# Kernel optimization log

Hardware: AMD Instinct MI355X
Metric: run time of the kernel (lower is better)

## Reference

```python
import jax, jax.numpy as jnp
import numpy as np

# Module dims (match init_kwargs)
D_IN = 1024
N_PRI = 2048
D_PRI = 16
N_CLS = 25
D_CLS = 16
ITERS = 3
B = 64
EPS = 1e-6


def layer_norm(x, g, b, eps=1e-5):
    m = x.mean(-1, keepdims=True)
    v = ((x - m) ** 2).mean(-1, keepdims=True)
    return (x - m) / jnp.sqrt(v + eps) * g + b


def setup_inputs() -> dict:
    key = jax.random.key(0)
    ks = jax.random.split(key, 6)
    s = lambda n: 1.0 / np.sqrt(n)
    return {
        "z": jax.random.normal(ks[0], (B, D_IN), jnp.float32),
        # to_primary: Linear(d_in, n_primary*d_primary)
        "w1": jax.random.normal(ks[1], (D_IN, N_PRI * D_PRI), jnp.float32) * s(D_IN),
        "b1": jnp.zeros((N_PRI * D_PRI,), jnp.float32),
        # primary_act: LayerNorm(d_in) -> Linear(d_in, n_primary) -> Sigmoid
        "ln1_g": jnp.ones((D_IN,), jnp.float32),
        "ln1_b": jnp.zeros((D_IN,), jnp.float32),
        "w2": jax.random.normal(ks[2], (D_IN, N_PRI), jnp.float32) * s(D_IN),
        "b2": jnp.zeros((N_PRI,), jnp.float32),
        # CapsuleFC transform + EM routing params
        "w_caps": jax.random.normal(ks[3], (N_PRI, D_PRI, N_CLS, D_CLS), jnp.float32) * s(D_PRI),
        "beta_u": jnp.zeros((N_CLS,), jnp.float32),
        "beta_a": jnp.zeros((N_CLS,), jnp.float32),
        # to_logits: LayerNorm(d_class) -> Linear(d_class, 1)
        "ln2_g": jnp.ones((D_CLS,), jnp.float32),
        "ln2_b": jnp.zeros((D_CLS,), jnp.float32),
        "w3": jax.random.normal(ks[4], (D_CLS, 1), jnp.float32) * s(D_CLS),
        "b3": jnp.zeros((1,), jnp.float32),
    }


def em_routing(V, a_in, beta_u, beta_a, n_iter):
    # V: (b, n_in, n_out, d) votes; a_in: (b, n_in) primary activations
    b, n, o, d = V.shape
    R = jnp.full((b, n, o), 1.0 / o, V.dtype)  # routing assignments
    lam = jnp.asarray(1.0, V.dtype)            # inverse temperature
    for _ in range(n_iter):
        # M-step: weighted mean/variance per output capsule
        r = R * a_in[:, :, None]                                  # (b,n,o)
        r_sum = r.sum(axis=1) + EPS                               # (b,o)
        mu = jnp.einsum('bno,bnod->bod', r, V) / r_sum[..., None]  # (b,o,d)
        diff2 = (V - mu[:, None]) ** 2                            # (b,n,o,d)
        sigma2 = jnp.einsum('bno,bnod->bod', r, diff2) / r_sum[..., None] + EPS
        cost = (beta_u[None, :, None] + 0.5 * jnp.log(sigma2)) * r_sum[..., None]
        a_out = jax.nn.sigmoid(lam * (beta_a[None, :] - cost.sum(-1)))  # (b,o)
        # E-step: Gaussian log-likelihood of each vote under each output capsule
        logp = (-0.5 * (diff2 / sigma2[:, None]).sum(-1)
                - 0.5 * jnp.log(sigma2).sum(-1)[:, None, :])      # (b,n,o)
        R = jax.nn.softmax(jnp.log(a_out + EPS)[:, None, :] + logp, axis=-1)
    return mu, a_out, R


def reference(z, w1, b1, ln1_g, ln1_b, w2, b2, w_caps, beta_u, beta_a,
              ln2_g, ln2_b, w3, b3):
    b = z.shape[0]
    # primary poses (no squash: use_squash_primary=False)
    primary_pose = (z @ w1 + b1).reshape(b, N_PRI, D_PRI)
    # primary activations
    primary_act = jnp.clip(jax.nn.sigmoid(layer_norm(z, ln1_g, ln1_b) @ w2 + b2), 0.0, 1.0)
    # votes: each primary capsule predicts each class capsule's pose
    V = jnp.einsum('bni,niod->bnod', primary_pose, w_caps)  # (B, N_PRI, N_CLS, D_CLS)
    class_pose, class_act, q = em_routing(V, primary_act, beta_u, beta_a, ITERS)
    logits = (layer_norm(class_pose, ln2_g, ln2_b) @ w3 + b3).squeeze(-1)  # (B, N_CLS)
    acts = jnp.linalg.norm(class_pose, axis=-1)                            # (B, N_CLS)
    return logits, acts, class_pose, q
```

## Files before the change

kernel.cpp:

```cpp
#include <hip/hip_runtime.h>
#include <hip/hip_bf16.h>
#include <cstdio>

#define B     64
#define DIN   1024
#define NPRI  2048
#define DPRI  16
#define NCLS  25
#define DCLS  16
#define EMEPS 1e-6f
#define LNEPS 1e-5f
#define KS2   8
#define NCHUNK_S 16

#define OFF_POSE 0
#define OFF_ZN   (OFF_POSE + NPRI*DPRI*B)
#define OFF_ACTT (OFF_ZN + B*DIN)
#define OFF_G2P  (OFF_ACTT + NPRI*B)
#define OFF_V    (OFF_G2P + KS2*NPRI*B)
#define V_FLOATS (NPRI*NCLS*B*DCLS/2)
#define OFF_R    (OFF_V + V_FLOATS)
#define R_FLOATS (NPRI*NCLS*B/2)
#define OFF_PART (OFF_R + R_FLOATS)
#define OFF_STAT (OFF_PART + NCLS*NCHUNK_S*33*B)
#define OFF_MU   (OFF_STAT + NCLS*33*B)
#define OFF_MI4  (OFF_MU + NCLS*DCLS*B)
#define OFF_BASE (OFF_MI4 + NCLS*8*B*4)
#define WS_FLOATS (OFF_BASE + NCLS*B)

__device__ __forceinline__ unsigned pack_f16(float a, float b) {
  union { _Float16 h[2]; unsigned u; } x;
  x.h[0] = (_Float16)a; x.h[1] = (_Float16)b;
  return x.u;
}
__device__ __forceinline__ float f16lo(unsigned u) {
  union { unsigned u; _Float16 h[2]; } x; x.u = u; return (float)x.h[0];
}
__device__ __forceinline__ float f16hi(unsigned u) {
  union { unsigned u; _Float16 h[2]; } x; x.u = u; return (float)x.h[1];
}
__device__ __forceinline__ unsigned short f16bits(float a) {
  union { _Float16 h; unsigned short u; } x; x.h = (_Float16)a; return x.u;
}
__device__ __forceinline__ float f16val(unsigned short u) {
  union { unsigned short u; _Float16 h; } x; x.u = u; return (float)x.h;
}

__global__ __launch_bounds__(256) void k_ln(const float* __restrict__ z,
                                            const float* __restrict__ g,
                                            const float* __restrict__ bb,
                                            float* __restrict__ zn) {
  int row = blockIdx.x, t = threadIdx.x;
  const float* zr = z + row * DIN;
  float4 v = ((const float4*)zr)[t];
  float s  = v.x + v.y + v.z + v.w;
  float s2 = v.x*v.x + v.y*v.y + v.z*v.z + v.w*v.w;
  for (int off = 32; off; off >>= 1) {
    s  += __shfl_down(s, off);
    s2 += __shfl_down(s2, off);
  }
  __shared__ float ls[8];
  int wv = t >> 6, ln = t & 63;
  if (ln == 0) { ls[wv*2] = s; ls[wv*2+1] = s2; }
  __syncthreads();
  s  = ls[0] + ls[2] + ls[4] + ls[6];
  s2 = ls[1] + ls[3] + ls[5] + ls[7];
  float mean = s * (1.0f / DIN);
  float var  = s2 * (1.0f / DIN) - mean * mean;
  float inv  = 1.0f / sqrtf(var + LNEPS);
  float4 gg = ((const float4*)g)[t];
  float4 bv = ((const float4*)bb)[t];
  float4 o;
  o.x = (v.x - mean) * inv * gg.x + bv.x;
  o.y = (v.y - mean) * inv * gg.y + bv.y;
  o.z = (v.z - mean) * inv * gg.z + bv.z;
  o.w = (v.w - mean) * inv * gg.w + bv.w;
  ((float4*)(zn + row * DIN))[t] = o;
}

__global__ __launch_bounds__(256, 2) void k_gemm1(const float* __restrict__ z,
                                                  const float* __restrict__ w1,
                                                  const float* __restrict__ b1,
                                                  float* __restrict__ poseT) {
  __shared__ __align__(16) float zTl[128 * 68];
  __shared__ __align__(16) float wl[128 * 68];
  int t = threadIdx.x;
  int c0 = blockIdx.x * 64;

  int r0  = (t >> 4) * 4;
  int c0l = (t & 15) * 4;

  int zr_ = t >> 2, za = t & 3;
  int wk = t >> 1, wc = (t & 1) * 32;

  float acc[4][4];
#pragma unroll
  for (int j = 0; j < 4; ++j)
#pragma unroll
    for (int i = 0; i < 4; ++i) acc[j][i] = 0.f;

  for (int kc = 0; kc < 8; ++kc) {
    int k0 = kc * 128;
    __syncthreads();
#pragma unroll
    for (int jj = 0; jj < 4; ++jj) {
      int kb = za * 8 + jj * 32;
      const float* src = z + zr_ * DIN + k0 + kb;
      float4 v0 = *(const float4*)src;
      float4 v1 = *(const float4*)(src + 4);
      zTl[(kb+0)*68 + zr_] = v0.x; zTl[(kb+1)*68 + zr_] = v0.y;
      zTl[(kb+2)*68 + zr_] = v0.z; zTl[(kb+3)*68 + zr_] = v0.w;
      zTl[(kb+4)*68 + zr_] = v1.x; zTl[(kb+5)*68 + zr_] = v1.y;
      zTl[(kb+6)*68 + zr_] = v1.z; zTl[(kb+7)*68 + zr_] = v1.w;
    }
    const float* wsrc = w1 + (size_t)(k0 + wk) * 32768 + c0 + wc;
#pragma unroll
    for (int j = 0; j < 8; ++j)
      *(float4*)&wl[wk * 68 + wc + j * 4] = *(const float4*)(wsrc + j * 4);
    __syncthreads();

#pragma unroll 4
    for (int k = 0; k < 128; ++k) {
      float4 zr4 = *(const float4*)&zTl[k * 68 + r0];
      float4 wr4 = *(const float4*)&wl[k * 68 + c0l];
      float zz[4] = {zr4.x, zr4.y, zr4.z, zr4.w};
      float ww[4] = {wr4.x, wr4.y, wr4.z, wr4.w};
#pragma unroll
      for (int j = 0; j < 4; ++j)
#pragma unroll
        for (int i = 0; i < 4; ++i) acc[j][i] += ww[j] * zz[i];
    }
  }
#pragma unroll
  for (int j = 0; j < 4; ++j) {
    int c = c0 + c0l + j;
    float bc = b1[c];
    float4 o = {acc[j][0] + bc, acc[j][1] + bc, acc[j][2] + bc, acc[j][3] + bc};
    *(float4*)&poseT[c * 64 + r0] = o;
  }
}

__global__ __launch_bounds__(256, 2) void k_gemm2p(const float* __restrict__ zn,
                                                   const float* __restrict__ w2,
                                                   float* __restrict__ part) {
  __shared__ __align__(16) float znT[128 * 68];
  __shared__ __align__(16) float wl[128 * 68];
  int t = threadIdx.x;
  int c0 = blockIdx.x * 64;
  int k0 = blockIdx.y * 128;
  int zr_ = t >> 2, za = t & 3;
  int wk = t >> 1, wc = (t & 1) * 32;

#pragma unroll
  for (int jj = 0; jj < 4; ++jj) {
    int kb = za * 8 + jj * 32;
    const float* src = zn + zr_ * DIN + k0 + kb;
    float4 v0 = *(const float4*)src;
    float4 v1 = *(const float4*)(src + 4);
    znT[(kb+0)*68 + zr_] = v0.x; znT[(kb+1)*68 + zr_] = v0.y;
    znT[(kb+2)*68 + zr_] = v0.z; znT[(kb+3)*68 + zr_] = v0.w;
    znT[(kb+4)*68 + zr_] = v1.x; znT[(kb+5)*68 + zr_] = v1.y;
    znT[(kb+6)*68 + zr_] = v1.z; znT[(kb+7)*68 + zr_] = v1.w;
  }
  const float* wsrc = w2 + (size_t)(k0 + wk) * NPRI + c0 + wc;
#pragma unroll
  for (int j = 0; j < 8; ++j)
    *(float4*)&wl[wk * 68 + wc + j * 4] = *(const float4*)(wsrc + j * 4);
  __syncthreads();

  int r0 = (t >> 4) * 4, c0l = (t & 15) * 4;
  float acc[4][4];
#pragma unroll
  for (int j = 0; j < 4; ++j)
#pragma unroll
    for (int i = 0; i < 4; ++i) acc[j][i] = 0.f;

#pragma unroll 4
  for (int k = 0; k < 128; ++k) {
    float4 z4 = *(const float4*)&znT[k * 68 + r0];
    float4 w4 = *(const float4*)&wl[k * 68 + c0l];
    float zz[4] = {z4.x, z4.y, z4.z, z4.w};
    float ww[4] = {w4.x, w4.y, w4.z, w4.w};
#pragma unroll
    for (int j = 0; j < 4; ++j)
#pragma unroll
      for (int i = 0; i < 4; ++i) acc[j][i] += ww[j] * zz[i];
  }
  float* pdst = part + ((size_t)blockIdx.y * NPRI + c0 + c0l) * 64 + r0;
#pragma unroll
  for (int j = 0; j < 4; ++j) {
    float4 o = {acc[j][0], acc[j][1], acc[j][2], acc[j][3]};
    *(float4*)&pdst[j * 64] = o;
  }
}

__global__ __launch_bounds__(256) void k_gemm2r(const float* __restrict__ part,
                                                const float* __restrict__ b2,
                                                float* __restrict__ actt) {
  int idx = blockIdx.x * 256 + threadIdx.x;
  float4 s = {0.f, 0.f, 0.f, 0.f};
#pragma unroll
  for (int kz = 0; kz < KS2; ++kz) {
    float4 v = *(const float4*)&part[(size_t)kz * NPRI * 64 + idx * 4];
    s.x += v.x; s.y += v.y; s.z += v.z; s.w += v.w;
  }
  int c = (idx * 4) >> 6;
  float bc = b2[c];
  float4 o;
  o.x = fminf(fmaxf(1.0f / (1.0f + expf(-(s.x + bc))), 0.0f), 1.0f);
  o.y = fminf(fmaxf(1.0f / (1.0f + expf(-(s.y + bc))), 0.0f), 1.0f);
  o.z = fminf(fmaxf(1.0f / (1.0f + expf(-(s.z + bc))), 0.0f), 1.0f);
  o.w = fminf(fmaxf(1.0f / (1.0f + expf(-(s.w + bc))), 0.0f), 1.0f);
  *(float4*)&actt[idx * 4] = o;
}

__global__ __launch_bounds__(256) void k_votes(const float* __restrict__ poseT,
                                               const float* __restrict__ wcaps,
                                               unsigned* __restrict__ V) {
  __shared__ __align__(16) float wl[6400];
  __shared__ __align__(16) float pl[64 * 16];
  int n = blockIdx.x, t = threadIdx.x;
  const float* wsrc = wcaps + (size_t)n * 6400;
  for (int idx = t * 4; idx < 6400; idx += 1024)
    *(float4*)(wl + idx) = *(const float4*)(wsrc + idx);
  {
    float4 v = *(const float4*)(poseT + n * 1024 + t * 4);
    int i = (t * 4) >> 6, b = (t * 4) & 63;
    pl[(b+0)*16 + i] = v.x; pl[(b+1)*16 + i] = v.y;
    pl[(b+2)*16 + i] = v.z; pl[(b+3)*16 + i] = v.w;
  }
  __syncthreads();
  if (t >= 200) return;
  int o = t / 8, d0 = (t % 8) * 2;
  float w0[16], w1_[16];
#pragma unroll
  for (int i = 0; i < 16; ++i) {
    w0[i]  = wl[(i * 25 + o) * 16 + d0];
    w1_[i] = wl[(i * 25 + o) * 16 + d0 + 1];
  }
  unsigned* vd = V + (((size_t)n * 25 + o) * 64 * 16 + d0) / 2;
  for (int b = 0; b < 64; ++b) {
    const float* pb = &pl[b * 16];
    float a0 = 0.f, a1 = 0.f;
#pragma unroll
    for (int i = 0; i < 16; ++i) {
      float p = pb[i];
      a0 += p * w0[i];
      a1 += p * w1_[i];
    }
    vd[b * 8] = pack_f16(a0, a1);
  }
}

template <bool UNIFORM>
__global__ __launch_bounds__(256) void k_stats(const unsigned* __restrict__ V,
                                               const float* __restrict__ actt,
                                               const unsigned short* __restrict__ Rh,
                                               float* __restrict__ part) {
  int o = blockIdx.y;
  int t = threadIdx.x, b = t & 63, wv = t >> 6;
  float S0 = 0.f, S1[16], S2[16];
#pragma unroll
  for (int d = 0; d < 16; ++d) { S1[d] = 0.f; S2[d] = 0.f; }
  int n0 = blockIdx.x * 128 + wv * 32;
  for (int k = 0; k < 32; ++k) {
    int n = n0 + k;
    float a = actt[n * 64 + b];
    float r = UNIFORM ? a * (1.0f / 25.0f)
                      : f16val(Rh[((size_t)n * 25 + o) * 64 + b]) * a;
    const uint4* vp = (const uint4*)(V + (((size_t)n * 25 + o) * 64 + b) * 8);
    uint4 u0 = vp[0], u1 = vp[1];
    unsigned uu[8] = {u0.x, u0.y, u0.z, u0.w, u1.x, u1.y, u1.z, u1.w};
    S0 += r;
#pragma unroll
    for (int q = 0; q < 8; ++q) {
      float v0 = f16lo(uu[q]), v1 = f16hi(uu[q]);
      float t0 = r * v0, t1 = r * v1;
      S1[2*q]   += t0;          S1[2*q+1] += t1;
      S2[2*q]   += t0 * v0;     S2[2*q+1] += t1 * v1;
    }
  }
  __shared__ float red[4 * 33 * 64];
  red[(wv * 33 + 0) * 64 + b] = S0;
#pragma unroll
  for (int d = 0; d < 16; ++d) {
    red[(wv * 33 + 1 + d) * 64 + b]  = S1[d];
    red[(wv * 33 + 17 + d) * 64 + b] = S2[d];
  }
  __syncthreads();
  if (wv == 0) {
    for (int s = 0; s < 33; ++s) {
      float tot = red[s * 64 + b] + red[(33 + s) * 64 + b] +
                  red[(66 + s) * 64 + b] + red[(99 + s) * 64 + b];
      part[((o * NCHUNK_S + blockIdx.x) * 33 + s) * 64 + b] = tot;
    }
  }
}

__global__ __launch_bounds__(256) void k_reduce(const float* __restrict__ part,
                                                float* __restrict__ stats) {
  int o = blockIdx.x;
  for (int idx = threadIdx.x; idx < 33 * 64; idx += 256) {
    float s = 0.f;
#pragma unroll
    for (int c = 0; c < NCHUNK_S; ++c)
      s += part[(o * NCHUNK_S + c) * 33 * 64 + idx];
    stats[o * 33 * 64 + idx] = s;
  }
}

__global__ __launch_bounds__(64) void k_finish(const float* __restrict__ stats,
                                               const float* __restrict__ beta_u,
                                               const float* __restrict__ beta_a,
                                               float* __restrict__ mu,
                                               float* __restrict__ mi4,
                                               float* __restrict__ basew) {
  int o = blockIdx.x, b = threadIdx.x;
  const float* st = stats + o * 33 * 64;
  float s0 = st[b];
  float rs = s0 + EMEPS;
  float inv_rs = 1.0f / rs;
  float ldet = 0.f;
  float mloc[16], iloc[16];
#pragma unroll
  for (int d = 0; d < 16; ++d) {
    float s1 = st[(1 + d) * 64 + b];
    float s2 = st[(17 + d) * 64 + b];
    float m = s1 * inv_rs;
    float var = (s2 - 2.0f * m * s1 + m * m * s0) * inv_rs;
    float sg = fmaxf(var, 0.0f) + EMEPS;
    mloc[d] = m;
    iloc[d] = 1.0f / sg;
    mu[(o * 16 + d) * 64 + b] = m;
    ldet += logf(sg);
  }
#pragma unroll
  for (int q = 0; q < 8; ++q) {
    float4 v = {mloc[2*q], iloc[2*q], mloc[2*q+1], iloc[2*q+1]};
    *(float4*)&mi4[((o * 8 + q) * 64 + b) * 4] = v;
  }
  float cost = (16.0f * beta_u[o] + 0.5f * ldet) * rs;
  float x = beta_a[o] - cost;
  float a = 1.0f / (1.0f + expf(-x));
  basew[o * 64 + b] = logf(a + EMEPS) - 0.5f * ldet;
}

template <bool FINAL>
__global__ __launch_bounds__(256) void k_estep(const unsigned* __restrict__ V,
                                               const float* __restrict__ mi4,
                                               const float* __restrict__ basew,
                                               unsigned short* __restrict__ Rh,
                                               float* __restrict__ qout) {
  int t = threadIdx.x, b = t & 63, ng = t >> 6;
  int n = blockIdx.x * 4 + ng;
  float l[25];
  float mx = -1e30f;
#pragma unroll
  for (int o = 0; o < 25; ++o) {
    const uint4* vp = (const uint4*)(V + (((size_t)n * 25 + o) * 64 + b) * 8);
    uint4 u0 = vp[0], u1 = vp[1];
    unsigned uu[8] = {u0.x, u0.y, u0.z, u0.w, u1.x, u1.y, u1.z, u1.w};
    float acc = 0.f;
#pragma unroll
    for (int qq = 0; qq < 8; ++qq) {
      float4 mi = *(const float4*)&mi4[((o * 8 + qq) * 64 + b) * 4];
      float d0 = f16lo(uu[qq]) - mi.x;
      float d1 = f16hi(uu[qq]) - mi.z;
      acc += d0 * d0 * mi.y + d1 * d1 * mi.w;
    }
    l[o] = basew[o * 64 + b] - 0.5f * acc;
    mx = fmaxf(mx, l[o]);
  }
  float s = 0.f;
#pragma unroll
  for (int o = 0; o < 25; ++o) { l[o] = expf(l[o] - mx); s += l[o]; }
  float inv = 1.0f / s;
  if (FINAL) {
    float* qp = qout + ((size_t)b * NPRI + n) * 25;
#pragma unroll
    for (int o = 0; o < 25; ++o) qp[o] = l[o] * inv;
  } else {
#pragma unroll
    for (int o = 0; o < 25; ++o)
      Rh[((size_t)n * 25 + o) * 64 + b] = f16bits(l[o] * inv);
  }
}

__global__ __launch_bounds__(64) void k_out(const float* __restrict__ mu,
                                            const float* __restrict__ g2,
                                            const float* __restrict__ bb2,
                                            const float* __restrict__ w3,
                                            const float* __restrict__ b3,
                                            float* __restrict__ out) {
  int o = blockIdx.x, b = threadIdx.x;
  float m[16];
  float s = 0.f;
#pragma unroll
  for (int d = 0; d < 16; ++d) { m[d] = mu[(o * 16 + d) * 64 + b]; s += m[d]; }
  float mean = s * (1.0f / 16.0f);
  float var = 0.f;
#pragma unroll
  for (int d = 0; d < 16; ++d) { float dd = m[d] - mean; var += dd * dd; }
  var *= (1.0f / 16.0f);
  float inv = 1.0f / sqrtf(var + LNEPS);
  float logit = 0.f, nrm = 0.f;
#pragma unroll
  for (int d = 0; d < 16; ++d) {
    float nh = (m[d] - mean) * inv * g2[d] + bb2[d];
    logit += nh * w3[d];
    nrm += m[d] * m[d];
  }
  out[b * 25 + o] = logit + b3[0];
  out[1600 + b * 25 + o] = sqrtf(nrm);
  float* pp = out + 3200 + (b * 25 + o) * 16;
#pragma unroll
  for (int d = 0; d < 16; ++d) pp[d] = m[d];
}

extern "C" void kernel_launch(void* const* d_in, const int* in_sizes, int n_in,
                              void* d_out, int out_size, void* d_ws, size_t ws_size,
                              hipStream_t stream) {
  const float* z      = (const float*)d_in[0];
  const float* w1     = (const float*)d_in[1];
  const float* b1     = (const float*)d_in[2];
  const float* ln1g   = (const float*)d_in[3];
  const float* ln1b   = (const float*)d_in[4];
  const float* w2     = (const float*)d_in[5];
  const float* b2     = (const float*)d_in[6];
  const float* wcaps  = (const float*)d_in[7];
  const float* beta_u = (const float*)d_in[8];
  const float* beta_a = (const float*)d_in[9];
  const float* ln2g   = (const float*)d_in[10];
  const float* ln2b   = (const float*)d_in[11];
  const float* w3     = (const float*)d_in[12];
  const float* b3     = (const float*)d_in[13];

  if (ws_size < (size_t)WS_FLOATS * 4) {
    fprintf(stderr, "kernel_launch: ws too small: %zu < %zu bytes\n",
            ws_size, (size_t)WS_FLOATS * 4);
  }

  float* ws    = (float*)d_ws;
  float* out   = (float*)d_out;
  float* poseT = ws + OFF_POSE;
  float* zn    = ws + OFF_ZN;
  float* actt  = ws + OFF_ACTT;
  float* g2p   = ws + OFF_G2P;
  unsigned* V  = (unsigned*)(ws + OFF_V);
  unsigned short* Rh = (unsigned short*)(ws + OFF_R);
  float* part  = ws + OFF_PART;
  float* st    = ws + OFF_STAT;
  float* muw   = ws + OFF_MU;
  float* mi4   = ws + OFF_MI4;
  float* bse   = ws + OFF_BASE;

  k_ln<<<64, 256, 0, stream>>>(z, ln1g, ln1b, zn);
  k_gemm1<<<512, 256, 0, stream>>>(z, w1, b1, poseT);
  k_gemm2p<<<dim3(32, KS2), 256, 0, stream>>>(zn, w2, g2p);
  k_gemm2r<<<128, 256, 0, stream>>>(g2p, b2, actt);
  k_votes<<<2048, 256, 0, stream>>>(poseT, wcaps, V);

  k_stats<true><<<dim3(NCHUNK_S, 25), 256, 0, stream>>>(V, actt, Rh, part);
  k_reduce<<<25, 256, 0, stream>>>(part, st);
  k_finish<<<25, 64, 0, stream>>>(st, beta_u, beta_a, muw, mi4, bse);

  for (int it = 0; it < 2; ++it) {
    k_estep<false><<<512, 256, 0, stream>>>(V, mi4, bse, Rh, nullptr);
    k_stats<false><<<dim3(NCHUNK_S, 25), 256, 0, stream>>>(V, actt, Rh, part);
    k_reduce<<<25, 256, 0, stream>>>(part, st);
    k_finish<<<25, 64, 0, stream>>>(st, beta_u, beta_a, muw, mi4, bse);
  }

  k_estep<true><<<512, 256, 0, stream>>>(V, mi4, bse, nullptr, out + 28800);
  k_out<<<25, 64, 0, stream>>>(muw, ln2g, ln2b, w3, b3, out);
}
```

Baseline: 392.3 us.

## Run primary pose GEMM on fp16 MFMA with pre-converted z

Result: slower. 422.6 us (+7.7%).

```diff
diff --git a/kernel.cpp b/kernel.cpp
--- a/kernel.cpp
+++ b/kernel.cpp
@@ -26,7 +26,11 @@
 #define OFF_MU   (OFF_STAT + NCLS*33*B)
 #define OFF_MI4  (OFF_MU + NCLS*DCLS*B)
 #define OFF_BASE (OFF_MI4 + NCLS*8*B*4)
-#define WS_FLOATS (OFF_BASE + NCLS*B)
+#define OFF_ZH   (OFF_BASE + NCLS*B)
+#define WS_FLOATS (OFF_ZH + B*DIN/2)
+
+typedef __attribute__((ext_vector_type(8))) _Float16 f16x8;
+typedef __attribute__((ext_vector_type(4))) float f32x4;
 
 __device__ __forceinline__ unsigned pack_f16(float a, float b) {
   union { _Float16 h[2]; unsigned u; } x;
@@ -44,6 +48,13 @@
 }
 __device__ __forceinline__ float f16val(unsigned short u) {
   union { unsigned short u; _Float16 h; } x; x.u = u; return (float)x.h;
+}
+
+__global__ __launch_bounds__(256) void k_zh(const float* __restrict__ z,
+                                            unsigned* __restrict__ zh) {
+  int idx = blockIdx.x * 256 + threadIdx.x;
+  float2 v = ((const float2*)z)[idx];
+  zh[idx] = pack_f16(v.x, v.y);
 }
 
 __global__ __launch_bounds__(256) void k_ln(const float* __restrict__ z,
@@ -78,65 +89,68 @@
   ((float4*)(zn + row * DIN))[t] = o;
 }
 
-__global__ __launch_bounds__(256, 2) void k_gemm1(const float* __restrict__ z,
-                                                  const float* __restrict__ w1,
-                                                  const float* __restrict__ b1,
-                                                  float* __restrict__ poseT) {
-  __shared__ __align__(16) float zTl[128 * 68];
-  __shared__ __align__(16) float wl[128 * 68];
+__global__ __launch_bounds__(256) void k_gemm1m(const unsigned* __restrict__ zh,
+                                                const float* __restrict__ w1,
+                                                const float* __restrict__ b1,
+                                                float* __restrict__ poseT) {
+  __shared__ __align__(16) unsigned bt[64 * 68];
   int t = threadIdx.x;
   int c0 = blockIdx.x * 64;
-
-  int r0  = (t >> 4) * 4;
-  int c0l = (t & 15) * 4;
-
-  int zr_ = t >> 2, za = t & 3;
-  int wk = t >> 1, wc = (t & 1) * 32;
-
-  float acc[4][4];
-#pragma unroll
-  for (int j = 0; j < 4; ++j)
-#pragma unroll
-    for (int i = 0; i < 4; ++i) acc[j][i] = 0.f;
+  int l = t & 63, w = t >> 6;
+  int colw = w * 16 + (l & 15);
+  int kq = l >> 4;
+
+  f32x4 acc0 = {0,0,0,0}, acc1 = {0,0,0,0}, acc2 = {0,0,0,0}, acc3 = {0,0,0,0};
+
+  int sc = t & 63;
+  int kp0 = t >> 6;
 
   for (int kc = 0; kc < 8; ++kc) {
     int k0 = kc * 128;
     __syncthreads();
 #pragma unroll
-    for (int jj = 0; jj < 4; ++jj) {
-      int kb = za * 8 + jj * 32;
-      const float* src = z + zr_ * DIN + k0 + kb;
-      float4 v0 = *(const float4*)src;
-      float4 v1 = *(const float4*)(src + 4);
-      zTl[(kb+0)*68 + zr_] = v0.x; zTl[(kb+1)*68 + zr_] = v0.y;
-      zTl[(kb+2)*68 + zr_] = v0.z; zTl[(kb+3)*68 + zr_] = v0.w;
-      zTl[(kb+4)*68 + zr_] = v1.x; zTl[(kb+5)*68 + zr_] = v1.y;
-      zTl[(kb+6)*68 + zr_] = v1.z; zTl[(kb+7)*68 + zr_] = v1.w;
-    }
-    const float* wsrc = w1 + (size_t)(k0 + wk) * 32768 + c0 + wc;
-#pragma unroll
-    for (int j = 0; j < 8; ++j)
-      *(float4*)&wl[wk * 68 + wc + j * 4] = *(const float4*)(wsrc + j * 4);
+    for (int i = 0; i < 16; ++i) {
+      int kp = kp0 + 4 * i;
+      int k = k0 + 2 * kp;
+      float v0 = w1[(size_t)k * 32768 + c0 + sc];
+      float v1 = w1[(size_t)(k + 1) * 32768 + c0 + sc];
+      bt[sc * 68 + kp] = pack_f16(v0, v1);
+    }
     __syncthreads();
-
-#pragma unroll 4
-    for (int k = 0; k < 128; ++k) {
-      float4 zr4 = *(const float4*)&zTl[k * 68 + r0];
-      float4 wr4 = *(const float4*)&wl[k * 68 + c0l];
-      float zz[4] = {zr4.x, zr4.y, zr4.z, zr4.w};
-      float ww[4] = {wr4.x, wr4.y, wr4.z, wr4.w};
-#pragma unroll
-      for (int j = 0; j < 4; ++j)
-#pragma unroll
-        for (int i = 0; i < 4; ++i) acc[j][i] += ww[j] * zz[i];
-    }
-  }
-#pragma unroll
-  for (int j = 0; j < 4; ++j) {
-    int c = c0 + c0l + j;
-    float bc = b1[c];
-    float4 o = {acc[j][0] + bc, acc[j][1] + bc, acc[j][2] + bc, acc[j][3] + bc};
-    *(float4*)&poseT[c * 64 + r0] = o;
+#pragma unroll
+    for (int ks = 0; ks < 4; ++ks) {
+      union { uint4 u; f16x8 h; } bc_;
+      bc_.u = *(const uint4*)&bt[colw * 68 + ks * 16 + kq * 4];
+#pragma unroll
+      for (int rc = 0; rc < 4; ++rc) {
+        int row = rc * 16 + (l & 15);
+        union { uint4 u; f16x8 h; } ac_;
+        ac_.u = *(const uint4*)&zh[((size_t)row * DIN + k0 + ks * 32 + kq * 8) >> 1];
+        if (rc == 0) acc0 = __builtin_amdgcn_mfma_f32_16x16x32_f16(ac_.h, bc_.h, acc0, 0, 0, 0);
+        if (rc == 1) acc1 = __builtin_amdgcn_mfma_f32_16x16x32_f16(ac_.h, bc_.h, acc1, 0, 0, 0);
+        if (rc == 2) acc2 = __builtin_amdgcn_mfma_f32_16x16x32_f16(ac_.h, bc_.h, acc2, 0, 0, 0);
+        if (rc == 3) acc3 = __builtin_amdgcn_mfma_f32_16x16x32_f16(ac_.h, bc_.h, acc3, 0, 0, 0);
+      }
+    }
+  }
+  int c = c0 + colw;
+  float bc = b1[c];
+  float* pdst = poseT + (size_t)c * 64 + kq * 4;
+  {
+    float4 o = {acc0[0] + bc, acc0[1] + bc, acc0[2] + bc, acc0[3] + bc};
+    *(float4*)&pdst[0] = o;
+  }
+  {
+    float4 o = {acc1[0] + bc, acc1[1] + bc, acc1[2] + bc, acc1[3] + bc};
+    *(float4*)&pdst[16] = o;
+  }
+  {
+    float4 o = {acc2[0] + bc, acc2[1] + bc, acc2[2] + bc, acc2[3] + bc};
+    *(float4*)&pdst[32] = o;
+  }
+  {
+    float4 o = {acc3[0] + bc, acc3[1] + bc, acc3[2] + bc, acc3[3] + bc};
+    *(float4*)&pdst[48] = o;
   }
 }
 
@@ -453,9 +467,11 @@
   float* muw   = ws + OFF_MU;
   float* mi4   = ws + OFF_MI4;
   float* bse   = ws + OFF_BASE;
-
+  unsigned* zh = (unsigned*)(ws + OFF_ZH);
+
+  k_zh<<<128, 256, 0, stream>>>(z, zh);
   k_ln<<<64, 256, 0, stream>>>(z, ln1g, ln1b, zn);
-  k_gemm1<<<512, 256, 0, stream>>>(z, w1, b1, poseT);
+  k_gemm1m<<<512, 256, 0, stream>>>(zh, w1, b1, poseT);
   k_gemm2p<<<dim3(32, KS2), 256, 0, stream>>>(zn, w2, g2p);
   k_gemm2r<<<128, 256, 0, stream>>>(g2p, b2, actt);
   k_votes<<<2048, 256, 0, stream>>>(poseT, wcaps, V);
```
